# Kernel optimization log

Hardware: AMD Instinct MI355X
Metric: run time of the kernel (lower is better)

The kernel has to match this reference:

```python
import jax, jax.numpy as jnp
import numpy as np

B, C, H, W = 8, 512, 32, 32
HEADS, GROUPS = 8, 32
EPS = 1e-5


def setup_inputs() -> dict:
    key = jax.random.key(0)
    ks = jax.random.split(key, 6)
    s = 0.02
    return {
        "x": jax.random.normal(ks[0], (B, C, H, W), jnp.float32),
        "gn_scale": jnp.ones((C,), jnp.float32),
        "gn_bias": jnp.zeros((C,), jnp.float32),
        "wq": jax.random.normal(ks[1], (C, C), jnp.float32) * s,
        "bq": jnp.zeros((C,), jnp.float32),
        "wk": jax.random.normal(ks[2], (C, C), jnp.float32) * s,
        "bk": jnp.zeros((C,), jnp.float32),
        "wv": jax.random.normal(ks[3], (C, C), jnp.float32) * s,
        "bv": jnp.zeros((C,), jnp.float32),
        "wo": jax.random.normal(ks[4], (C, C), jnp.float32) * s,
        "bo": jnp.zeros((C,), jnp.float32),
    }


def reference(x, gn_scale, gn_bias, wq, bq, wk, bk, wv, bv, wo, bo):
    b, c, h, w = x.shape
    n = h * w
    cdh = c // HEADS
    xf = x.reshape(b, c, n)

    # GroupNorm over (channels_per_group, spatial)
    g = xf.reshape(b, GROUPS, (c // GROUPS) * n)
    mu = g.mean(-1, keepdims=True)
    var = g.var(-1, keepdims=True)
    hn = ((g - mu) * jax.lax.rsqrt(var + EPS)).reshape(b, c, n)
    hn = hn * gn_scale[:, None] + gn_bias[:, None]

    # 1x1 conv projections == channel-mixing GEMMs
    q = jnp.einsum('oc,bcn->bon', wq, hn) + bq[:, None]
    k = jnp.einsum('oc,bcn->bon', wk, hn) + bk[:, None]
    v = jnp.einsum('oc,bcn->bon', wv, hn) + bv[:, None]

    qh = q.reshape(b, HEADS, cdh, n)
    kh = k.reshape(b, HEADS, cdh, n)
    vh = v.reshape(b, HEADS, cdh, n)

    scale = 1.0 / jnp.sqrt(jnp.float32(cdh))
    scores = jnp.einsum('bhdq,bhdk->bhqk', qh, kh) * scale  # [B,H,N,N]
    attn = jax.nn.softmax(scores, axis=-1)  # dropout p=0.0 (eval) -> identity

    oh = jnp.einsum('bhqk,bhdk->bhdq', attn, vh).reshape(b, c, n)
    out = jnp.einsum('oc,bcn->bon', wo, oh) + bo[:, None]
    return (xf + out).reshape(b, c, h, w)
```

## Files before the change

### kernel.cpp

```cpp
#include <hip/hip_runtime.h>

#define BB 8
#define CC 512
#define NSP 1024
#define HEADS 8
#define DH 64
#define NGROUPS 32
#define CPG 16
#define GN_EPS 1e-5f
#define MQKV 1536

typedef __attribute__((ext_vector_type(8))) short bf16x8;
typedef __attribute__((ext_vector_type(4))) short short4v;
typedef __attribute__((ext_vector_type(4))) float f32x4;

typedef __attribute__((address_space(3))) unsigned int lds_u32;
typedef const __attribute__((address_space(1))) unsigned int glb_u32;

__device__ __forceinline__ short f2bf(float f) {
    union { float f; unsigned u; } v; v.f = f;
    unsigned r = v.u + 0x7fffu + ((v.u >> 16) & 1u);
    return (short)(r >> 16);
}
__device__ __forceinline__ short f2bf_trunc(float f) {
    union { float f; unsigned u; } v; v.f = f;
    return (short)(v.u >> 16);
}

__device__ __forceinline__ float wave_reduce_sum(float v) {
    #pragma unroll
    for (int off = 32; off > 0; off >>= 1) v += __shfl_down(v, off, 64);
    return v;
}

#define QSCALE 0.18033688011112042f

__global__ __launch_bounds__(256) void gn_conv_kernel(
        const float* __restrict__ x, const float* __restrict__ gsc,
        const float* __restrict__ gbi, short* __restrict__ hnt,
        const float* __restrict__ wq, const float* __restrict__ wk,
        const float* __restrict__ wv, const float* __restrict__ wo,
        const float* __restrict__ bq, const float* __restrict__ bk,
        const float* __restrict__ bv,
        short* __restrict__ wqkv, short* __restrict__ wob,
        float* __restrict__ bqkv) {
    __shared__ float xs[CPG * NSP];
    __shared__ float red[2][4];
    const int t = threadIdx.x;

    if (blockIdx.x >= 256) {
        const int base = (blockIdx.x - 256) * 1024 + t * 4;
        short pk[4];
        if (base < MQKV * CC) {
            const int r = base >> 9, cc = base & 511;
            const float* src = (r < 512) ? wq : ((r < 1024) ? wk : wv);
            float4 v = *(const float4*)&src[(size_t)(r & 511) * CC + cc];
            if (r < 512) { v.x *= QSCALE; v.y *= QSCALE; v.z *= QSCALE; v.w *= QSCALE; }
            pk[0] = f2bf(v.x); pk[1] = f2bf(v.y); pk[2] = f2bf(v.z); pk[3] = f2bf(v.w);
            *(short4v*)&wqkv[base] = *(short4v*)pk;
        } else {
            const int g2 = base - MQKV * CC;
            float4 v = *(const float4*)&wo[g2];
            pk[0] = f2bf(v.x); pk[1] = f2bf(v.y); pk[2] = f2bf(v.z); pk[3] = f2bf(v.w);
            *(short4v*)&wob[g2] = *(short4v*)pk;
        }
        const int fid = (blockIdx.x - 256) * 256 + t;
        if (fid < MQKV) {
            float bvv = (fid < 512) ? bq[fid] * QSCALE
                      : ((fid < 1024) ? bk[fid - 512] : bv[fid - 1024]);
            bqkv[fid] = bvv;
        }
        return;
    }

    const int b = blockIdx.x >> 5, g = blockIdx.x & 31;
    const int count = CPG * NSP;
    const size_t base = ((size_t)b * CC + (size_t)g * CPG) * NSP;
    float s = 0.f, ss = 0.f;
    for (int i = t * 4; i < count; i += 1024) {
        float4 v = *(const float4*)&x[base + i];
        *(float4*)&xs[i] = v;
        s += v.x + v.y + v.z + v.w;
        ss += v.x * v.x + v.y * v.y + v.z * v.z + v.w * v.w;
    }
    s = wave_reduce_sum(s); ss = wave_reduce_sum(ss);
    const int wid = t >> 6, lane = t & 63;
    if (lane == 0) { red[0][wid] = s; red[1][wid] = ss; }
    __syncthreads();
    if (t == 0) {
        float ts  = red[0][0] + red[0][1] + red[0][2] + red[0][3];
        float tss = red[1][0] + red[1][1] + red[1][2] + red[1][3];
        float mu = ts / count;
        float var = tss / count - mu * mu;
        red[0][0] = mu;
        red[1][0] = rsqrtf(var + GN_EPS);
    }
    __syncthreads();
    const float mu = red[0][0], rstd = red[1][0];
    float sc[16], bi[16];
    #pragma unroll
    for (int ci = 0; ci < 16; ++ci) {
        sc[ci] = gsc[g * CPG + ci] * rstd;
        bi[ci] = gbi[g * CPG + ci];
    }
    for (int n0 = 0; n0 < NSP; n0 += 256) {
        const int n = n0 + t;
        short tmp[16];
        #pragma unroll
        for (int ci = 0; ci < 16; ++ci) {
            float v = xs[ci * NSP + n];
            tmp[ci] = f2bf((v - mu) * sc[ci] + bi[ci]);
        }
        const size_t ob = ((size_t)b * NSP + n) * CC + g * CPG;
        *(bf16x8*)&hnt[ob]     = *(bf16x8*)&tmp[0];
        *(bf16x8*)&hnt[ob + 8] = *(bf16x8*)&tmp[8];
    }
}

template <int MODE>
__global__ __launch_bounds__(256) void gemm_bt_kernel(
        const short* __restrict__ A, const float* __restrict__ bias,
        const short* __restrict__ Bt, void* __restrict__ Yv,
        const float* __restrict__ res, short* __restrict__ qt,
        short* __restrict__ kt, int M) {
    __shared__ short As[64 * 64];
    __shared__ short Bs[128 * 64];
    const int nt = blockIdx.x;
    const int b = nt >> 3, n0 = (nt & 7) * 128;
    const int o0 = blockIdx.y * 64;
    const int t = threadIdx.x, w = t >> 6, lane = t & 63;
    const int quad = lane >> 4, l16 = lane & 15;

    f32x4 acc[4][2];
    #pragma unroll
    for (int i = 0; i < 4; ++i)
        #pragma unroll
        for (int j = 0; j < 2; ++j) acc[i][j] = (f32x4){0.f, 0.f, 0.f, 0.f};

    const short* Ab = A + (size_t)o0 * 512;
    const short* Bb = Bt + ((size_t)b * 1024 + n0) * 512;
    const int lrow = lane >> 3, lch = lane & 7;

    for (int k0 = 0; k0 < 512; k0 += 64) {
        #pragma unroll
        for (int p = 0; p < 2; ++p) {
            const int row = w * 16 + p * 8 + lrow;
            __builtin_amdgcn_global_load_lds(
                (glb_u32*)(Ab + (size_t)row * 512 + k0 + lch * 8),
                (lds_u32*)&As[(w * 2 + p) * 512], 16, 0, 0);
        }
        #pragma unroll
        for (int p = 0; p < 4; ++p) {
            const int row = w * 32 + p * 8 + lrow;
            __builtin_amdgcn_global_load_lds(
                (glb_u32*)(Bb + (size_t)row * 512 + k0 + lch * 8),
                (lds_u32*)&Bs[(w * 4 + p) * 512], 16, 0, 0);
        }
        __syncthreads();

        bf16x8 af[4][2], bfr[2][2];
        #pragma unroll
        for (int mi = 0; mi < 4; ++mi)
            #pragma unroll
            for (int s = 0; s < 2; ++s)
                af[mi][s] = *(bf16x8*)&As[(mi * 16 + l16) * 64 + quad * 8 + s * 32];
        #pragma unroll
        for (int ni = 0; ni < 2; ++ni)
            #pragma unroll
            for (int s = 0; s < 2; ++s)
                bfr[ni][s] = *(bf16x8*)&Bs[(w * 32 + ni * 16 + l16) * 64 + quad * 8 + s * 32];
        #pragma unroll
        for (int mi = 0; mi < 4; ++mi)
            #pragma unroll
            for (int ni = 0; ni < 2; ++ni)
                #pragma unroll
                for (int s = 0; s < 2; ++s)
                    acc[mi][ni] = __builtin_amdgcn_mfma_f32_16x16x32_bf16(
                        af[mi][s], bfr[ni][s], acc[mi][ni], 0, 0, 0);
        __syncthreads();
    }

    if (MODE == 0 && o0 < 1024) {
        short* T = (o0 < 512) ? qt : kt;
        const int hh = (o0 & 511) >> 6;
        const size_t hb2 = ((size_t)b * HEADS + hh) * NSP;
        short* Ts = Bs + w * 2048;
        #pragma unroll
        for (int mi = 0; mi < 4; ++mi) {
            const int d0 = mi * 16 + quad * 4;
            const int c = d0 >> 3, dlo = d0 & 7;
            float bv[4];
            #pragma unroll
            for (int r = 0; r < 4; ++r) bv[r] = bias[o0 + d0 + r];
            #pragma unroll
            for (int ni = 0; ni < 2; ++ni) {
                const int nl = ni * 16 + l16;
                short pk[4];
                #pragma unroll
                for (int r = 0; r < 4; ++r) pk[r] = f2bf(acc[mi][ni][r] + bv[r]);
                *(short4v*)&Ts[nl * 64 + ((c ^ (nl & 7)) * 8) + dlo] = *(short4v*)pk;
            }
        }
        #pragma unroll
        for (int it = 0; it < 4; ++it) {
            const int rr = lrow + it * 8;
            bf16x8 vv = *(bf16x8*)&Ts[rr * 64 + ((lch ^ (rr & 7)) * 8)];
            *(bf16x8*)&T[(hb2 + n0 + w * 32 + rr) * DH + lch * 8] = vv;
        }
        return;
    }

    #pragma unroll
    for (int mi = 0; mi < 4; ++mi) {
        #pragma unroll
        for (int r = 0; r < 4; ++r) {
            const int m = mi * 16 + quad * 4 + r;
            const float bv = bias[o0 + m];
            const size_t rowb = ((size_t)b * M + o0 + m) * 1024 + n0;
            if (MODE == 0) {
                short* Y = (short*)Yv;
                #pragma unroll
                for (int ni = 0; ni < 2; ++ni) {
                    const int n = w * 32 + ni * 16 + l16;
                    Y[rowb + n] = f2bf(acc[mi][ni][r] + bv);
                }
            } else {
                float* Y = (float*)Yv;
                #pragma unroll
                for (int ni = 0; ni < 2; ++ni) {
                    const int n = w * 32 + ni * 16 + l16;
                    Y[rowb + n] = acc[mi][ni][r] + bv + res[rowb + n];
                }
            }
        }
    }
}

__global__ __launch_bounds__(256) void attn_mfma_kernel(
        const short* __restrict__ qkv, const short* __restrict__ qt,
        const short* __restrict__ kt, short* __restrict__ obt) {
    __shared__ short Ks[64 * 64];
    __shared__ short Vs[64 * 64];
    __shared__ short Ps[4][32][68];
    const int id = blockIdx.x;
    const int xcd = id & 7, j = id >> 3;
    const int q0 = (j & 7) * 128;
    const int hi = (j >> 3) * 8 + xcd;
    const int b = hi >> 3, h = hi & 7;
    const int t = threadIdx.x;
    const int w = t >> 6, lane = t & 63;
    const int quad = lane >> 4, l16 = lane & 15;
    const size_t vbase = ((size_t)b * MQKV + 1024 + h * DH) * NSP;
    const size_t hb = ((size_t)b * HEADS + h) * NSP;
    const int sc = (lane & 7) ^ (lane >> 3);
    const int swz0 = (quad ^ (l16 & 7)) * 8;
    const int swz1 = ((quad + 4) ^ (l16 & 7)) * 8;

    bf16x8 qf[2][2];
    #pragma unroll
    for (int g = 0; g < 2; ++g)
        #pragma unroll
        for (int s = 0; s < 2; ++s)
            qf[g][s] = *(const bf16x8*)&qt[(hb + q0 + w * 32 + g * 16 + l16) * DH
                                           + quad * 8 + 32 * s];

    float lsum[2] = {0.f, 0.f};
    f32x4 oacc[2][4];
    #pragma unroll
    for (int g = 0; g < 2; ++g)
        #pragma unroll
        for (int i = 0; i < 4; ++i) oacc[g][i] = (f32x4){0.f, 0.f, 0.f, 0.f};

    for (int k0 = 0; k0 < NSP; k0 += 64) {
        __syncthreads();
        #pragma unroll
        for (int p = 0; p < 2; ++p) {
            const int row = w * 16 + p * 8 + (lane >> 3);
            __builtin_amdgcn_global_load_lds(
                (glb_u32*)(kt + (hb + k0 + row) * DH + sc * 8),
                (lds_u32*)(Ks + w * 1024 + p * 512), 16, 0, 0);
            __builtin_amdgcn_global_load_lds(
                (glb_u32*)(qkv + vbase + (size_t)row * NSP + k0 + sc * 8),
                (lds_u32*)(Vs + w * 1024 + p * 512), 16, 0, 0);
        }
        __syncthreads();

        f32x4 st[2][4];
        #pragma unroll
        for (int ks = 0; ks < 4; ++ks) {
            bf16x8 ka0 = *(bf16x8*)&Ks[(ks * 16 + l16) * 64 + swz0];
            bf16x8 ka1 = *(bf16x8*)&Ks[(ks * 16 + l16) * 64 + swz1];
            #pragma unroll
            for (int g = 0; g < 2; ++g) {
                f32x4 a2 = (f32x4){0.f, 0.f, 0.f, 0.f};
                a2 = __builtin_amdgcn_mfma_f32_16x16x32_bf16(ka0, qf[g][0], a2, 0, 0, 0);
                a2 = __builtin_amdgcn_mfma_f32_16x16x32_bf16(ka1, qf[g][1], a2, 0, 0, 0);
                st[g][ks] = a2;
            }
        }

        #pragma unroll
        for (int g = 0; g < 2; ++g) {
            short pb[16];
            #pragma unroll
            for (int ks = 0; ks < 4; ++ks)
                #pragma unroll
                for (int r = 0; r < 4; ++r) {
                    float p = exp2f(st[g][ks][r]);
                    lsum[g] += p;
                    pb[ks * 4 + r] = f2bf_trunc(p);
                }
            #pragma unroll
            for (int ks = 0; ks < 4; ++ks)
                *(short4v*)&Ps[w][g * 16 + l16][ks * 16 + quad * 4] = *(short4v*)&pb[ks * 4];
        }
        bf16x8 pf[2][2];
        #pragma unroll
        for (int g = 0; g < 2; ++g)
            #pragma unroll
            for (int s = 0; s < 2; ++s)
                pf[g][s] = *(bf16x8*)&Ps[w][g * 16 + l16][quad * 8 + 32 * s];

        #pragma unroll
        for (int ds = 0; ds < 4; ++ds) {
            bf16x8 va0 = *(bf16x8*)&Vs[(ds * 16 + l16) * 64 + swz0];
            bf16x8 va1 = *(bf16x8*)&Vs[(ds * 16 + l16) * 64 + swz1];
            #pragma unroll
            for (int g = 0; g < 2; ++g) {
                oacc[g][ds] = __builtin_amdgcn_mfma_f32_16x16x32_bf16(va0, pf[g][0], oacc[g][ds], 0, 0, 0);
                oacc[g][ds] = __builtin_amdgcn_mfma_f32_16x16x32_bf16(va1, pf[g][1], oacc[g][ds], 0, 0, 0);
            }
        }
    }

    #pragma unroll
    for (int g = 0; g < 2; ++g) {
        float ls = lsum[g];
        ls += __shfl_xor(ls, 16, 64);
        ls += __shfl_xor(ls, 32, 64);
        const float inv = 1.0f / ls;
        const int qrow = q0 + w * 32 + g * 16 + l16;
        #pragma unroll
        for (int ds = 0; ds < 4; ++ds) {
            short o4[4];
            #pragma unroll
            for (int r = 0; r < 4; ++r) o4[r] = f2bf(oacc[g][ds][r] * inv);
            *(short4v*)&obt[((size_t)b * NSP + qrow) * CC + h * DH + ds * 16 + quad * 4] =
                *(short4v*)o4;
        }
    }
}

extern "C" void kernel_launch(void* const* d_in, const int* in_sizes, int n_in,
                              void* d_out, int out_size, void* d_ws, size_t ws_size,
                              hipStream_t stream) {
    const float* x   = (const float*)d_in[0];
    const float* gsc = (const float*)d_in[1];
    const float* gbi = (const float*)d_in[2];
    const float* wq  = (const float*)d_in[3];
    const float* bq  = (const float*)d_in[4];
    const float* wk  = (const float*)d_in[5];
    const float* bk  = (const float*)d_in[6];
    const float* wv  = (const float*)d_in[7];
    const float* bv  = (const float*)d_in[8];
    const float* wo  = (const float*)d_in[9];
    const float* bo  = (const float*)d_in[10];
    float* out = (float*)d_out;

    short* wqkv_bf = (short*)d_ws;
    short* wo_bf   = wqkv_bf + (size_t)MQKV * CC;
    float* bqkv    = (float*)(wo_bf + (size_t)CC * CC);
    short* hnt     = (short*)(bqkv + MQKV);
    short* qkv     = hnt + (size_t)BB * NSP * CC;
    short* obt     = qkv + (size_t)BB * MQKV * NSP;
    short* kt      = obt + (size_t)BB * NSP * CC;
    short* qt      = kt + (size_t)BB * HEADS * NSP * DH;

    gn_conv_kernel<<<1280, 256, 0, stream>>>(
        x, gsc, gbi, hnt, wq, wk, wv, wo, bq, bk, bv, wqkv_bf, wo_bf, bqkv);

    dim3 qkvgrid(64, MQKV / 64);
    gemm_bt_kernel<0><<<qkvgrid, 256, 0, stream>>>(
        wqkv_bf, bqkv, hnt, (void*)qkv, nullptr, qt, kt, MQKV);

    attn_mfma_kernel<<<512, 256, 0, stream>>>(qkv, qt, kt, obt);

    dim3 wogrid(64, CC / 64);
    gemm_bt_kernel<1><<<wogrid, 256, 0, stream>>>(
        wo_bf, bo, obt, (void*)out, x, nullptr, nullptr, CC);
}
```

Baseline: 165.8 us.

## Drop LDS staging in GEMM and attention, load MFMA fragments directly from global

Both the projection GEMM and the attention kernel stop staging tiles in shared memory with global_load_lds and barriers. Each wave now loads its MFMA operand fragments straight from global memory, relying on L1/L2 for reuse across waves. The QKV GEMM also gets a template parameter that makes each block compute two 128-column tiles, halving its grid. This removes barrier and LDS traffic but adds redundant global loads across waves and uses more accumulator registers.

Result: slower. 230.6 us (+39.1%).

```diff
diff --git a/kernel.cpp b/kernel.cpp
--- a/kernel.cpp
+++ b/kernel.cpp
@@ -13,9 +13,6 @@
 typedef __attribute__((ext_vector_type(8))) short bf16x8;
 typedef __attribute__((ext_vector_type(4))) short short4v;
 typedef __attribute__((ext_vector_type(4))) float f32x4;
-
-typedef __attribute__((address_space(3))) unsigned int lds_u32;
-typedef const __attribute__((address_space(1))) unsigned int glb_u32;
 
 __device__ __forceinline__ short f2bf(float f) {
     union { float f; unsigned u; } v; v.f = f;
@@ -117,119 +114,114 @@
     }
 }
 
-template <int MODE>
+template <int MODE, int NT>
 __global__ __launch_bounds__(256) void gemm_bt_kernel(
         const short* __restrict__ A, const float* __restrict__ bias,
         const short* __restrict__ Bt, void* __restrict__ Yv,
         const float* __restrict__ res, short* __restrict__ qt,
         short* __restrict__ kt, int M) {
-    __shared__ short As[64 * 64];
-    __shared__ short Bs[128 * 64];
+    __shared__ short Ts[4][2048];
+    const int NB = 8 / NT;
     const int nt = blockIdx.x;
-    const int b = nt >> 3, n0 = (nt & 7) * 128;
+    const int b = nt / NB, n0 = (nt % NB) * (128 * NT);
     const int o0 = blockIdx.y * 64;
     const int t = threadIdx.x, w = t >> 6, lane = t & 63;
     const int quad = lane >> 4, l16 = lane & 15;
-
-    f32x4 acc[4][2];
-    #pragma unroll
-    for (int i = 0; i < 4; ++i)
-        #pragma unroll
-        for (int j = 0; j < 2; ++j) acc[i][j] = (f32x4){0.f, 0.f, 0.f, 0.f};
+    const int lrow = lane >> 3, lch = lane & 7;
+
+    f32x4 acc[NT][4][2];
+    #pragma unroll
+    for (int tt = 0; tt < NT; ++tt)
+        #pragma unroll
+        for (int i = 0; i < 4; ++i)
+            #pragma unroll
+            for (int j = 0; j < 2; ++j) acc[tt][i][j] = (f32x4){0.f, 0.f, 0.f, 0.f};
 
     const short* Ab = A + (size_t)o0 * 512;
     const short* Bb = Bt + ((size_t)b * 1024 + n0) * 512;
-    const int lrow = lane >> 3, lch = lane & 7;
 
     for (int k0 = 0; k0 < 512; k0 += 64) {
-        #pragma unroll
-        for (int p = 0; p < 2; ++p) {
-            const int row = w * 16 + p * 8 + lrow;
-            __builtin_amdgcn_global_load_lds(
-                (glb_u32*)(Ab + (size_t)row * 512 + k0 + lch * 8),
-                (lds_u32*)&As[(w * 2 + p) * 512], 16, 0, 0);
-        }
-        #pragma unroll
-        for (int p = 0; p < 4; ++p) {
-            const int row = w * 32 + p * 8 + lrow;
-            __builtin_amdgcn_global_load_lds(
-                (glb_u32*)(Bb + (size_t)row * 512 + k0 + lch * 8),
-                (lds_u32*)&Bs[(w * 4 + p) * 512], 16, 0, 0);
-        }
-        __syncthreads();
-
-        bf16x8 af[4][2], bfr[2][2];
-        #pragma unroll
-        for (int mi = 0; mi < 4; ++mi)
-            #pragma unroll
-            for (int s = 0; s < 2; ++s)
-                af[mi][s] = *(bf16x8*)&As[(mi * 16 + l16) * 64 + quad * 8 + s * 32];
-        #pragma unroll
-        for (int ni = 0; ni < 2; ++ni)
-            #pragma unroll
-            for (int s = 0; s < 2; ++s)
-                bfr[ni][s] = *(bf16x8*)&Bs[(w * 32 + ni * 16 + l16) * 64 + quad * 8 + s * 32];
-        #pragma unroll
-        for (int mi = 0; mi < 4; ++mi)
-            #pragma unroll
-            for (int ni = 0; ni < 2; ++ni)
+        bf16x8 af[4][2];
+        #pragma unroll
+        for (int mi = 0; mi < 4; ++mi) {
+            const short* ar = Ab + (size_t)(mi * 16 + l16) * 512 + k0 + quad * 8;
+            af[mi][0] = *(const bf16x8*)ar;
+            af[mi][1] = *(const bf16x8*)(ar + 32);
+        }
+        #pragma unroll
+        for (int tt = 0; tt < NT; ++tt) {
+            #pragma unroll
+            for (int ni = 0; ni < 2; ++ni) {
+                const short* br = Bb + (size_t)(tt * 128 + w * 32 + ni * 16 + l16) * 512
+                                + k0 + quad * 8;
+                bf16x8 b0 = *(const bf16x8*)br;
+                bf16x8 b1 = *(const bf16x8*)(br + 32);
                 #pragma unroll
-                for (int s = 0; s < 2; ++s)
-                    acc[mi][ni] = __builtin_amdgcn_mfma_f32_16x16x32_bf16(
-                        af[mi][s], bfr[ni][s], acc[mi][ni], 0, 0, 0);
-        __syncthreads();
+                for (int mi = 0; mi < 4; ++mi) {
+                    acc[tt][mi][ni] = __builtin_amdgcn_mfma_f32_16x16x32_bf16(
+                        af[mi][0], b0, acc[tt][mi][ni], 0, 0, 0);
+                    acc[tt][mi][ni] = __builtin_amdgcn_mfma_f32_16x16x32_bf16(
+                        af[mi][1], b1, acc[tt][mi][ni], 0, 0, 0);
+                }
+            }
+        }
     }
 
     if (MODE == 0 && o0 < 1024) {
         short* T = (o0 < 512) ? qt : kt;
         const int hh = (o0 & 511) >> 6;
         const size_t hb2 = ((size_t)b * HEADS + hh) * NSP;
-        short* Ts = Bs + w * 2048;
-        #pragma unroll
-        for (int mi = 0; mi < 4; ++mi) {
-            const int d0 = mi * 16 + quad * 4;
-            const int c = d0 >> 3, dlo = d0 & 7;
-            float bv[4];
-            #pragma unroll
-            for (int r = 0; r < 4; ++r) bv[r] = bias[o0 + d0 + r];
-            #pragma unroll
-            for (int ni = 0; ni < 2; ++ni) {
-                const int nl = ni * 16 + l16;
-                short pk[4];
+        #pragma unroll
+        for (int tt = 0; tt < NT; ++tt) {
+            #pragma unroll
+            for (int mi = 0; mi < 4; ++mi) {
+                const int d0 = mi * 16 + quad * 4;
+                const int c = d0 >> 3, dlo = d0 & 7;
+                float bv[4];
                 #pragma unroll
-                for (int r = 0; r < 4; ++r) pk[r] = f2bf(acc[mi][ni][r] + bv[r]);
-                *(short4v*)&Ts[nl * 64 + ((c ^ (nl & 7)) * 8) + dlo] = *(short4v*)pk;
-            }
-        }
-        #pragma unroll
-        for (int it = 0; it < 4; ++it) {
-            const int rr = lrow + it * 8;
-            bf16x8 vv = *(bf16x8*)&Ts[rr * 64 + ((lch ^ (rr & 7)) * 8)];
-            *(bf16x8*)&T[(hb2 + n0 + w * 32 + rr) * DH + lch * 8] = vv;
-        }
-        return;
-    }
-
-    #pragma unroll
-    for (int mi = 0; mi < 4; ++mi) {
-        #pragma unroll
-        for (int r = 0; r < 4; ++r) {
-            const int m = mi * 16 + quad * 4 + r;
-            const float bv = bias[o0 + m];
-            const size_t rowb = ((size_t)b * M + o0 + m) * 1024 + n0;
-            if (MODE == 0) {
-                short* Y = (short*)Yv;
+                for (int r = 0; r < 4; ++r) bv[r] = bias[o0 + d0 + r];
                 #pragma unroll
                 for (int ni = 0; ni < 2; ++ni) {
-                    const int n = w * 32 + ni * 16 + l16;
-                    Y[rowb + n] = f2bf(acc[mi][ni][r] + bv);
+                    const int nl = ni * 16 + l16;
+                    short pk[4];
+                    #pragma unroll
+                    for (int r = 0; r < 4; ++r) pk[r] = f2bf(acc[tt][mi][ni][r] + bv[r]);
+                    *(short4v*)&Ts[w][nl * 64 + ((c ^ (nl & 7)) * 8) + dlo] = *(short4v*)pk;
                 }
-            } else {
-                float* Y = (float*)Yv;
-                #pragma unroll
-                for (int ni = 0; ni < 2; ++ni) {
-                    const int n = w * 32 + ni * 16 + l16;
-                    Y[rowb + n] = acc[mi][ni][r] + bv + res[rowb + n];
+            }
+            #pragma unroll
+            for (int it = 0; it < 4; ++it) {
+                const int rr = lrow + it * 8;
+                bf16x8 vv = *(bf16x8*)&Ts[w][rr * 64 + ((lch ^ (rr & 7)) * 8)];
+                *(bf16x8*)&T[(hb2 + n0 + tt * 128 + w * 32 + rr) * DH + lch * 8] = vv;
+            }
+        }
+        return;
+    }
+
+    #pragma unroll
+    for (int tt = 0; tt < NT; ++tt) {
+        #pragma unroll
+        for (int mi = 0; mi < 4; ++mi) {
+            #pragma unroll
+            for (int r = 0; r < 4; ++r) {
+                const int m = mi * 16 + quad * 4 + r;
+                const float bv = bias[o0 + m];
+                const size_t rowb = ((size_t)b * M + o0 + m) * 1024 + n0 + tt * 128;
+                if (MODE == 0) {
+                    short* Y = (short*)Yv;
+                    #pragma unroll
+                    for (int ni = 0; ni < 2; ++ni) {
+                        const int n = w * 32 + ni * 16 + l16;
+                        Y[rowb + n] = f2bf(acc[tt][mi][ni][r] + bv);
+                    }
+                } else {
+                    float* Y = (float*)Yv;
+                    #pragma unroll
+                    for (int ni = 0; ni < 2; ++ni) {
+                        const int n = w * 32 + ni * 16 + l16;
+                        Y[rowb + n] = acc[tt][mi][ni][r] + bv + res[rowb + n];
+                    }
                 }
             }
         }
@@ -239,8 +231,6 @@
 __global__ __launch_bounds__(256) void attn_mfma_kernel(
         const short* __restrict__ qkv, const short* __restrict__ qt,
         const short* __restrict__ kt, short* __restrict__ obt) {
-    __shared__ short Ks[64 * 64];
-    __shared__ short Vs[64 * 64];
     __shared__ short Ps[4][32][68];
     const int id = blockIdx.x;
     const int xcd = id & 7, j = id >> 3;
@@ -252,9 +242,6 @@
     const int quad = lane >> 4, l16 = lane & 15;
     const size_t vbase = ((size_t)b * MQKV + 1024 + h * DH) * NSP;
     const size_t hb = ((size_t)b * HEADS + h) * NSP;
-    const int sc = (lane & 7) ^ (lane >> 3);
-    const int swz0 = (quad ^ (l16 & 7)) * 8;
-    const int swz1 = ((quad + 4) ^ (l16 & 7)) * 8;
 
     bf16x8 qf[2][2];
     #pragma unroll
@@ -272,24 +259,12 @@
         for (int i = 0; i < 4; ++i) oacc[g][i] = (f32x4){0.f, 0.f, 0.f, 0.f};
 
     for (int k0 = 0; k0 < NSP; k0 += 64) {
-        __syncthreads();
-        #pragma unroll
-        for (int p = 0; p < 2; ++p) {
-            const int row = w * 16 + p * 8 + (lane >> 3);
-            __builtin_amdgcn_global_load_lds(
-                (glb_u32*)(kt + (hb + k0 + row) * DH + sc * 8),
-                (lds_u32*)(Ks + w * 1024 + p * 512), 16, 0, 0);
-            __builtin_amdgcn_global_load_lds(
-                (glb_u32*)(qkv + vbase + (size_t)row * NSP + k0 + sc * 8),
-                (lds_u32*)(Vs + w * 1024 + p * 512), 16, 0, 0);
-        }
-        __syncthreads();
-
         f32x4 st[2][4];
         #pragma unroll
         for (int ks = 0; ks < 4; ++ks) {
-            bf16x8 ka0 = *(bf16x8*)&Ks[(ks * 16 + l16) * 64 + swz0];
-            bf16x8 ka1 = *(bf16x8*)&Ks[(ks * 16 + l16) * 64 + swz1];
+            const short* kr = kt + (hb + k0 + ks * 16 + l16) * DH + quad * 8;
+            bf16x8 ka0 = *(const bf16x8*)kr;
+            bf16x8 ka1 = *(const bf16x8*)(kr + 32);
             #pragma unroll
             for (int g = 0; g < 2; ++g) {
                 f32x4 a2 = (f32x4){0.f, 0.f, 0.f, 0.f};
@@ -297,6 +272,14 @@
                 a2 = __builtin_amdgcn_mfma_f32_16x16x32_bf16(ka1, qf[g][1], a2, 0, 0, 0);
                 st[g][ks] = a2;
             }
+        }
+
+        bf16x8 va[4][2];
+        #pragma unroll
+        for (int ds = 0; ds < 4; ++ds) {
+            const short* vr = qkv + vbase + (size_t)(ds * 16 + l16) * NSP + k0 + quad * 8;
+            va[ds][0] = *(const bf16x8*)vr;
+            va[ds][1] = *(const bf16x8*)(vr + 32);
         }
 
         #pragma unroll
@@ -322,15 +305,14 @@
                 pf[g][s] = *(bf16x8*)&Ps[w][g * 16 + l16][quad * 8 + 32 * s];
 
         #pragma unroll
-        for (int ds = 0; ds < 4; ++ds) {
-            bf16x8 va0 = *(bf16x8*)&Vs[(ds * 16 + l16) * 64 + swz0];
-            bf16x8 va1 = *(bf16x8*)&Vs[(ds * 16 + l16) * 64 + swz1];
+        for (int ds = 0; ds < 4; ++ds)
             #pragma unroll
             for (int g = 0; g < 2; ++g) {
-                oacc[g][ds] = __builtin_amdgcn_mfma_f32_16x16x32_bf16(va0, pf[g][0], oacc[g][ds], 0, 0, 0);
-                oacc[g][ds] = __builtin_amdgcn_mfma_f32_16x16x32_bf16(va1, pf[g][1], oacc[g][ds], 0, 0, 0);
-            }
-        }
+                oacc[g][ds] = __builtin_amdgcn_mfma_f32_16x16x32_bf16(
+                    va[ds][0], pf[g][0], oacc[g][ds], 0, 0, 0);
+                oacc[g][ds] = __builtin_amdgcn_mfma_f32_16x16x32_bf16(
+                    va[ds][1], pf[g][1], oacc[g][ds], 0, 0, 0);
+            }
     }
 
     #pragma unroll
@@ -379,13 +361,13 @@
     gn_conv_kernel<<<1280, 256, 0, stream>>>(
         x, gsc, gbi, hnt, wq, wk, wv, wo, bq, bk, bv, wqkv_bf, wo_bf, bqkv);
 
-    dim3 qkvgrid(64, MQKV / 64);
-    gemm_bt_kernel<0><<<qkvgrid, 256, 0, stream>>>(
+    dim3 qkvgrid(32, 24);
+    gemm_bt_kernel<0, 2><<<qkvgrid, 256, 0, stream>>>(
         wqkv_bf, bqkv, hnt, (void*)qkv, nullptr, qt, kt, MQKV);
 
     attn_mfma_kernel<<<512, 256, 0, stream>>>(qkv, qt, kt, obt);
 
-    dim3 wogrid(64, CC / 64);
-    gemm_bt_kernel<1><<<wogrid, 256, 0, stream>>>(
+    dim3 wogrid(64, 8);
+    gemm_bt_kernel<1, 1><<<wogrid, 256, 0, stream>>>(
         wo_bf, bo, obt, (void*)out, x, nullptr, nullptr, CC);
 }
```

## Halve attention block to two waves, each owning 64 query rows

Applied to the files above, without the earlier changes.

The attention kernel now runs 128 threads per block. Each wave processes 64 query rows (4 groups of 16) instead of 32, so every K/V fragment read from LDS is reused across twice as many MFMAs. The K and V fragments for a tile are loaded into registers once, and the P staging buffer shrinks to one 16-row slab per wave, reused for each group. This cuts LDS reads and block count per tile but raises register pressure, halves the waves per block, and serialises the P round-trip per group, which may reduce latency hiding.

After: 186.7 us. 12.6% more time.

```diff
diff --git a/kernel.cpp b/kernel.cpp
--- a/kernel.cpp
+++ b/kernel.cpp
@@ -236,12 +236,12 @@
     }
 }
 
-__global__ __launch_bounds__(256) void attn_mfma_kernel(
+__global__ __launch_bounds__(128, 2) void attn_mfma_kernel(
         const short* __restrict__ qkv, const short* __restrict__ qt,
         const short* __restrict__ kt, short* __restrict__ obt) {
     __shared__ short Ks[64 * 64];
     __shared__ short Vs[64 * 64];
-    __shared__ short Ps[4][32][68];
+    __shared__ short Ps[2][16][68];
     const int id = blockIdx.x;
     const int xcd = id & 7, j = id >> 3;
     const int q0 = (j & 7) * 128;
@@ -256,90 +256,86 @@
     const int swz0 = (quad ^ (l16 & 7)) * 8;
     const int swz1 = ((quad + 4) ^ (l16 & 7)) * 8;
 
-    bf16x8 qf[2][2];
-    #pragma unroll
-    for (int g = 0; g < 2; ++g)
+    bf16x8 qf[4][2];
+    #pragma unroll
+    for (int g = 0; g < 4; ++g)
         #pragma unroll
         for (int s = 0; s < 2; ++s)
-            qf[g][s] = *(const bf16x8*)&qt[(hb + q0 + w * 32 + g * 16 + l16) * DH
+            qf[g][s] = *(const bf16x8*)&qt[(hb + q0 + w * 64 + g * 16 + l16) * DH
                                            + quad * 8 + 32 * s];
 
-    float lsum[2] = {0.f, 0.f};
-    f32x4 oacc[2][4];
-    #pragma unroll
-    for (int g = 0; g < 2; ++g)
+    float lsum[4] = {0.f, 0.f, 0.f, 0.f};
+    f32x4 oacc[4][4];
+    #pragma unroll
+    for (int g = 0; g < 4; ++g)
         #pragma unroll
         for (int i = 0; i < 4; ++i) oacc[g][i] = (f32x4){0.f, 0.f, 0.f, 0.f};
 
     for (int k0 = 0; k0 < NSP; k0 += 64) {
         __syncthreads();
         #pragma unroll
-        for (int p = 0; p < 2; ++p) {
-            const int row = w * 16 + p * 8 + (lane >> 3);
+        for (int p = 0; p < 4; ++p) {
+            const int row = w * 32 + p * 8 + (lane >> 3);
             __builtin_amdgcn_global_load_lds(
                 (glb_u32*)(kt + (hb + k0 + row) * DH + sc * 8),
-                (lds_u32*)(Ks + w * 1024 + p * 512), 16, 0, 0);
+                (lds_u32*)(Ks + (w * 32 + p * 8) * 64), 16, 0, 0);
             __builtin_amdgcn_global_load_lds(
                 (glb_u32*)(qkv + vbase + (size_t)row * NSP + k0 + sc * 8),
-                (lds_u32*)(Vs + w * 1024 + p * 512), 16, 0, 0);
+                (lds_u32*)(Vs + (w * 32 + p * 8) * 64), 16, 0, 0);
         }
         __syncthreads();
 
-        f32x4 st[2][4];
+        bf16x8 ka[4][2], va[4][2];
         #pragma unroll
         for (int ks = 0; ks < 4; ++ks) {
-            bf16x8 ka0 = *(bf16x8*)&Ks[(ks * 16 + l16) * 64 + swz0];
-            bf16x8 ka1 = *(bf16x8*)&Ks[(ks * 16 + l16) * 64 + swz1];
-            #pragma unroll
-            for (int g = 0; g < 2; ++g) {
+            ka[ks][0] = *(bf16x8*)&Ks[(ks * 16 + l16) * 64 + swz0];
+            ka[ks][1] = *(bf16x8*)&Ks[(ks * 16 + l16) * 64 + swz1];
+            va[ks][0] = *(bf16x8*)&Vs[(ks * 16 + l16) * 64 + swz0];
+            va[ks][1] = *(bf16x8*)&Vs[(ks * 16 + l16) * 64 + swz1];
+        }
+
+        #pragma unroll
+        for (int g = 0; g < 4; ++g) {
+            f32x4 st[4];
+            #pragma unroll
+            for (int ks = 0; ks < 4; ++ks) {
                 f32x4 a2 = (f32x4){0.f, 0.f, 0.f, 0.f};
-                a2 = __builtin_amdgcn_mfma_f32_16x16x32_bf16(ka0, qf[g][0], a2, 0, 0, 0);
-                a2 = __builtin_amdgcn_mfma_f32_16x16x32_bf16(ka1, qf[g][1], a2, 0, 0, 0);
-                st[g][ks] = a2;
+                a2 = __builtin_amdgcn_mfma_f32_16x16x32_bf16(ka[ks][0], qf[g][0], a2, 0, 0, 0);
+                a2 = __builtin_amdgcn_mfma_f32_16x16x32_bf16(ka[ks][1], qf[g][1], a2, 0, 0, 0);
+                st[ks] = a2;
             }
-        }
-
-        #pragma unroll
-        for (int g = 0; g < 2; ++g) {
             short pb[16];
             #pragma unroll
             for (int ks = 0; ks < 4; ++ks)
                 #pragma unroll
                 for (int r = 0; r < 4; ++r) {
-                    float p = exp2f(st[g][ks][r]);
+                    float p = exp2f(st[ks][r]);
                     lsum[g] += p;
                     pb[ks * 4 + r] = f2bf_trunc(p);
                 }
             #pragma unroll
             for (int ks = 0; ks < 4; ++ks)
-                *(short4v*)&Ps[w][g * 16 + l16][ks * 16 + quad * 4] = *(short4v*)&pb[ks * 4];
-        }
-        bf16x8 pf[2][2];
-        #pragma unroll
-        for (int g = 0; g < 2; ++g)
-            #pragma unroll
-            for (int s = 0; s < 2; ++s)
-                pf[g][s] = *(bf16x8*)&Ps[w][g * 16 + l16][quad * 8 + 32 * s];
-
-        #pragma unroll
-        for (int ds = 0; ds < 4; ++ds) {
-            bf16x8 va0 = *(bf16x8*)&Vs[(ds * 16 + l16) * 64 + swz0];
-            bf16x8 va1 = *(bf16x8*)&Vs[(ds * 16 + l16) * 64 + swz1];
-            #pragma unroll
-            for (int g = 0; g < 2; ++g) {
-                oacc[g][ds] = __builtin_amdgcn_mfma_f32_16x16x32_bf16(va0, pf[g][0], oacc[g][ds], 0, 0, 0);
-                oacc[g][ds] = __builtin_amdgcn_mfma_f32_16x16x32_bf16(va1, pf[g][1], oacc[g][ds], 0, 0, 0);
+                *(short4v*)&Ps[w][l16][ks * 16 + quad * 4] = *(short4v*)&pb[ks * 4];
+            bf16x8 pf0 = *(bf16x8*)&Ps[w][l16][quad * 8];
+            bf16x8 pf1 = *(bf16x8*)&Ps[w][l16][quad * 8 + 32];
+
+            #pragma unroll
+            for (int ds = 0; ds < 4; ++ds) {
+                oacc[g][ds] = __builtin_amdgcn_mfma_f32_16x16x32_bf16(
+                    va[ds][0], pf0, oacc[g][ds], 0, 0, 0);
+                oacc[g][ds] = __builtin_amdgcn_mfma_f32_16x16x32_bf16(
+                    va[ds][1], pf1, oacc[g][ds], 0, 0, 0);
             }
         }
     }
 
     #pragma unroll
-    for (int g = 0; g < 2; ++g) {
+    for (int g = 0; g < 4; ++g) {
         float ls = lsum[g];
         ls += __shfl_xor(ls, 16, 64);
         ls += __shfl_xor(ls, 32, 64);
         const float inv = 1.0f / ls;
-        const int qrow = q0 + w * 32 + g * 16 + l16;
+        const int qrow = q0 + w * 64 + g * 16 + l16;
         #pragma unroll
         for (int ds = 0; ds < 4; ++ds) {
             short o4[4];
@@ -383,7 +379,7 @@
     gemm_bt_kernel<0><<<qkvgrid, 256, 0, stream>>>(
         wqkv_bf, bqkv, hnt, (void*)qkv, nullptr, qt, kt, MQKV);
 
-    attn_mfma_kernel<<<512, 256, 0, stream>>>(qkv, qt, kt, obt);
+    attn_mfma_kernel<<<512, 128, 0, stream>>>(qkv, qt, kt, obt);
 
     dim3 wogrid(64, CC / 64);
     gemm_bt_kernel<1><<<wogrid, 256, 0, stream>>>(
```
